# Kernel optimization log

Hardware: AMD Instinct MI355X
Metric: run time of the kernel (lower is better)

The kernel has to match this reference:

```python
import jax, jax.numpy as jnp
import numpy as np

ENCODER_STRIDE = 320
TEMPERATURE = 1.0


def setup_inputs() -> dict:
    key = jax.random.key(0)
    k1, k2, k3, k4 = jax.random.split(key, 4)
    B, D, T, K = 8, 512, 4096, 4096
    student_features = jax.random.normal(k1, (B, D, T), dtype=jnp.float32)
    codebook = jax.random.normal(k2, (K, D), dtype=jnp.float32)
    teacher_codes = jax.random.randint(k3, (B, T), 0, K, dtype=jnp.int64)
    lengths = jax.random.randint(k4, (B,), 0, T * ENCODER_STRIDE, dtype=jnp.int64)
    return {
        "student_features": student_features,
        "codebook": codebook,
        "teacher_codes": teacher_codes,
        "lengths": lengths,
    }


def reference(student_features, codebook, teacher_codes, lengths):
    B, D, T = student_features.shape
    # length mask over frames: frame t is valid if its start sample < length
    frame_starts = jnp.arange(T, dtype=jnp.int64) * ENCODER_STRIDE  # [T]
    mask = (frame_starts[None, :] < lengths[:, None]).astype(student_features.dtype)  # [B,T]

    z = jnp.transpose(student_features, (0, 2, 1)).reshape(-1, D)  # [N,D], N=B*T

    # cdist p=2: sqrt(|z|^2 + |c|^2 - 2 z.c)
    z2 = jnp.sum(z * z, axis=1, keepdims=True)            # [N,1]
    c2 = jnp.sum(codebook * codebook, axis=1)[None, :]    # [1,K]
    d2 = z2 + c2 - 2.0 * (z @ codebook.T)                 # [N,K]
    dists = jnp.sqrt(jnp.maximum(d2, 1e-12))

    soft_weights = jax.nn.softmax(-dists / TEMPERATURE, axis=1)  # [N,K]
    soft_recon = soft_weights @ codebook                          # [N,D]

    codes_flat = teacher_codes.reshape(-1)                        # [N]
    target_embeddings = jax.lax.stop_gradient(codebook[codes_flat])  # [N,D]

    diff_sq = jnp.mean((soft_recon - target_embeddings) ** 2, axis=1).reshape(B, T)
    loss = jnp.sum(diff_sq * mask) / (jnp.sum(mask) + 1e-8)
    return loss
```

## Files before the change

kernel.cpp:

```cpp
#include <hip/hip_runtime.h>
#include <hip/hip_bf16.h>


#define BB 8
#define DD 512
#define TT 4096
#define KKK 4096
#define ENC_STRIDE 320
#define KT 32
#define NKT (KKK / KT)
#define NW 8
#define ROWS 128
#define KBROW 2056
#define KBBYTES 4112
#define BUFB (8 * KBBYTES)

typedef __attribute__((ext_vector_type(8))) short bf16x8;
typedef __attribute__((ext_vector_type(4))) float f32x4;

union FragU { bf16x8 v; uint2 h2[2]; ushort us[8]; unsigned long long q[2]; uint4 u4; };

static __device__ __forceinline__ ushort f2bf(float x) {
  unsigned u = __float_as_uint(x);
  unsigned r = (u + 0x7FFFu + ((u >> 16) & 1u)) >> 16;
  return (ushort)r;
}
static __device__ __forceinline__ uint2 f4tobf(float4 v) {
  uint2 r;
  r.x = (unsigned)f2bf(v.x) | ((unsigned)f2bf(v.y) << 16);
  r.y = (unsigned)f2bf(v.z) | ((unsigned)f2bf(v.w) << 16);
  return r;
}
static __device__ __forceinline__ unsigned pk2bf(float lo, float hi) {
  return (__float_as_uint(lo) >> 16) | (__float_as_uint(hi) & 0xFFFF0000u);
}
static __device__ __forceinline__ void gld_lds16(const void* g, void* l) {
  __builtin_amdgcn_global_load_lds(
      (const __attribute__((address_space(1))) unsigned*)g,
      (__attribute__((address_space(3))) unsigned*)l, 16, 0, 0);
}
static __device__ __forceinline__ unsigned lds_addr(const void* p) {
  return (unsigned)(size_t)(const __attribute__((address_space(3))) char*)p;
}

__global__ __launch_bounds__(256) void vq_prep(const float* __restrict__ cb,
                                               float* __restrict__ c2,
                                               ushort* __restrict__ cbh) {
  int k = blockIdx.x * 4 + (threadIdx.x >> 6);
  int lane = threadIdx.x & 63;
  const float4* p = (const float4*)(cb + (size_t)k * DD + lane * 8);
  float4 a = p[0], b = p[1];
  if (cbh) {
    uint2 pa = f4tobf(a), pb = f4tobf(b);
    *(uint4*)(cbh + (size_t)k * DD + lane * 8) = make_uint4(pa.x, pa.y, pb.x, pb.y);
  }
  float s = a.x*a.x + a.y*a.y + a.z*a.z + a.w*a.w
          + b.x*b.x + b.y*b.y + b.z*b.z + b.w*b.w;
  #pragma unroll
  for (int m = 1; m <= 32; m <<= 1) s += __shfl_xor(s, m);
  if (lane == 0) c2[k] = s;
}

template <int GLD>
__global__ __launch_bounds__(512, 2) void vq_main(
    const float* __restrict__ sf,
    const float* __restrict__ cb,
    const ushort* __restrict__ cbh,
    const int*  __restrict__ codes,
    const int*  __restrict__ lens,
    const float* __restrict__ c2,
    float* __restrict__ num) {
  __shared__ __align__(128) ushort cs[4][8][KBROW];
  __shared__ __align__(16) ushort wlds[2][NW][16][40];
  __shared__ float  alds[2][ROWS];
  __shared__ float  llds[ROWS];
  __shared__ float  diffred[ROWS];
  __shared__ int    flagv[NKT];

  const int bid = blockIdx.x;
  const int b  = bid >> 5;
  const int t0 = (bid & 31) << 7;
  const int len = lens[b];
  int vcount = (len + (ENC_STRIDE - 1)) / ENC_STRIDE;
  vcount = vcount < TT ? vcount : TT;
  if (t0 >= vcount) return;

  const int tid = threadIdx.x;
  const int w  = tid >> 6;
  const int l  = tid & 63;
  const int lg = l >> 4;
  const int ln = l & 15;

  for (int i = tid; i < ROWS; i += 512) diffred[i] = 0.f;
  for (int i = tid; i < NKT; i += 512) flagv[i] = 0;

  const float* sfb = sf + (size_t)b * DD * TT;
  const int trow = t0 + w * 16 + ln;
  bf16x8 za[16];
  float z2 = 0.f;
  #pragma unroll
  for (int f = 0; f < 16; ++f) {
    #pragma unroll
    for (int j = 0; j < 8; ++j) {
      int d = f * 32 + lg * 8 + j;
      float v = sfb[(size_t)d * TT + trow];
      z2 += v * v;
      za[f][j] = (short)f2bf(v);
    }
  }
  z2 += __shfl_xor(z2, 16);
  z2 += __shfl_xor(z2, 32);

  const int sbase = (w * 4 + ((l >> 1) & 3)) * DD + (l >> 3) * 16 + (l & 1) * 8;
  auto stage = [&](int kt, int buf) {
    if (GLD) {
      const ushort* gb = cbh + (size_t)kt * KT * DD + sbase;
      ushort* lb = &cs[buf][w][0];
      #pragma unroll
      for (int q = 0; q < 4; ++q) gld_lds16(gb + q * 128, lb + q * 512);
    } else {
      const float* gb = cb + (size_t)kt * KT * DD + sbase;
      #pragma unroll
      for (int q = 0; q < 4; ++q) {
        float4 v0 = *(const float4*)(gb + q * 128);
        float4 v1 = *(const float4*)(gb + q * 128 + 4);
        uint2 a0 = f4tobf(v0), a1 = f4tobf(v1);
        *(uint4*)&cs[buf][w][q * 512 + l * 8] = make_uint4(a0.x, a0.y, a1.x, a1.y);
      }
    }
  };

  stage(0, 0); stage(1, 1); stage(2, 2);

  float mrow = -1e30f, lrow = 0.f;
  f32x4 acc[8][4];
  #pragma unroll
  for (int r = 0; r < 8; ++r)
    #pragma unroll
    for (int nt = 0; nt < 4; ++nt) acc[r][nt] = (f32x4){0.f, 0.f, 0.f, 0.f};

  const unsigned score_lane = (unsigned)((ln >> 2) * KBBYTES + (ln & 3) * 32
                                         + (lg >> 1) * 128 + (lg & 1) * 16);
  const unsigned tr_lane = (unsigned)(lg * KBBYTES + w * 512 + ln * 8);
  const unsigned cs0a = lds_addr(&cs[0][0][0]);

  f32x4 sc0, sc1;
  auto scores = [&](int it, int sbuf) {
    const char* csb = (const char*)&cs[sbuf][0][0];
    sc0 = (f32x4){0,0,0,0}; sc1 = (f32x4){0,0,0,0};
    __builtin_amdgcn_s_setprio(1);
    #pragma unroll
    for (int f = 0; f < 16; ++f) {
      bf16x8 a0 = *(const bf16x8*)(csb + score_lane + f * 256);
      bf16x8 a1 = *(const bf16x8*)(csb + score_lane + 16448 + f * 256);
      sc0 = __builtin_amdgcn_mfma_f32_16x16x32_bf16(a0, za[f], sc0, 0, 0, 0);
      sc1 = __builtin_amdgcn_mfma_f32_16x16x32_bf16(a1, za[f], sc1, 0, 0, 0);
    }
    __builtin_amdgcn_s_setprio(0);
  };

  __syncthreads();
  scores(0, 0);
  {
    const float4 c2a = *(const float4*)(c2 + lg * 4);
    const float4 c2b = *(const float4*)(c2 + 16 + lg * 4);
    float c2v[8] = {c2a.x, c2a.y, c2a.z, c2a.w, c2b.x, c2b.y, c2b.z, c2b.w};
    float sv[8];
    #pragma unroll
    for (int v = 0; v < 4; ++v) {
      sv[v]     = -sqrtf(fmaxf(z2 + c2v[v]     - 2.f * sc0[v], 1e-12f));
      sv[4 + v] = -sqrtf(fmaxf(z2 + c2v[4 + v] - 2.f * sc1[v], 1e-12f));
    }
    float lmax = sv[0];
    #pragma unroll
    for (int i = 1; i < 8; ++i) lmax = fmaxf(lmax, sv[i]);
    float tmax = fmaxf(lmax, __shfl_xor(lmax, 16));
    tmax = fmaxf(tmax, __shfl_xor(tmax, 32));
    float el[8], lsum = 0.f;
    #pragma unroll
    for (int i = 0; i < 8; ++i) { el[i] = __expf(sv[i] - lmax); lsum += el[i]; }
    mrow = tmax;
    float factor = __expf(lmax - tmax);
    float esum = lsum * factor;
    esum += __shfl_xor(esum, 16);
    esum += __shfl_xor(esum, 32);
    lrow = esum;
    uint4 pk;
    pk.x = pk2bf(el[0] * factor, el[1] * factor);
    pk.y = pk2bf(el[2] * factor, el[3] * factor);
    pk.z = pk2bf(el[4] * factor, el[5] * factor);
    pk.w = pk2bf(el[6] * factor, el[7] * factor);
    *(uint4*)&wlds[0][w][ln][lg * 8] = pk;
    if (lg == 0) alds[0][w * 16 + ln] = 1.f;
  }

  #pragma unroll 1
  for (int it = 1; it < NKT; ++it) {
    __syncthreads();
    if (it + 2 < NKT) stage(it + 2, (it + 2) & 3);

    scores(it, it & 3);

    const float4 c2a = *(const float4*)(c2 + it * KT + lg * 4);
    const float4 c2b = *(const float4*)(c2 + it * KT + 16 + lg * 4);
    float c2v[8] = {c2a.x, c2a.y, c2a.z, c2a.w, c2b.x, c2b.y, c2b.z, c2b.w};
    float sv[8];
    #pragma unroll
    for (int v = 0; v < 4; ++v) {
      sv[v]     = -sqrtf(fmaxf(z2 + c2v[v]     - 2.f * sc0[v], 1e-12f));
      sv[4 + v] = -sqrtf(fmaxf(z2 + c2v[4 + v] - 2.f * sc1[v], 1e-12f));
    }
    float lmax = sv[0];
    #pragma unroll
    for (int i = 1; i < 8; ++i) lmax = fmaxf(lmax, sv[i]);
    float el[8], lsum = 0.f;
    #pragma unroll
    for (int i = 0; i < 8; ++i) { el[i] = __expf(sv[i] - lmax); lsum += el[i]; }

    const int itm1 = it - 1;
    const int s = itm1 & 1;
    const unsigned trb = cs0a + (unsigned)(itm1 & 3) * BUFB + tr_lane;
    unsigned long long tq0[4], tq1[4];
    #pragma unroll
    for (int nt = 0; nt < 4; ++nt) {
      asm volatile("ds_read_b64_tr_b16 %0, %2 offset:%3\n\t"
                   "ds_read_b64_tr_b16 %1, %2 offset:%4"
                   : "=&v"(tq0[nt]), "=&v"(tq1[nt])
                   : "v"(trb), "i"(nt * 128), "i"(16448 + nt * 128));
    }

    float tmax = fmaxf(lmax, __shfl_xor(lmax, 16));
    tmax = fmaxf(tmax, __shfl_xor(tmax, 32));
    const bool defer = (tmax <= mrow + 8.f);
    const float mnew = defer ? mrow : tmax;
    const float factor = __expf(lmax - mnew);
    float esum = lsum * factor;
    esum += __shfl_xor(esum, 16);
    esum += __shfl_xor(esum, 32);
    const float alpha = defer ? 1.f : __expf(mrow - mnew);
    lrow = lrow * alpha + esum;
    mrow = mnew;
    uint4 pk;
    pk.x = pk2bf(el[0] * factor, el[1] * factor);
    pk.y = pk2bf(el[2] * factor, el[3] * factor);
    pk.z = pk2bf(el[4] * factor, el[5] * factor);
    pk.w = pk2bf(el[6] * factor, el[7] * factor);
    const int s2 = it & 1;
    *(uint4*)&wlds[s2][w][ln][lg * 8] = pk;
    if (lg == 0) alds[s2][w * 16 + ln] = alpha;
    if (!__all(defer) && l == 0) flagv[it] = 1;

    const int flg = flagv[itm1];
    asm volatile("s_waitcnt lgkmcnt(0)" ::: "memory");
    __builtin_amdgcn_sched_barrier(0);

    if (flg) {
      #pragma unroll
      for (int r = 0; r < 8; ++r)
        #pragma unroll
        for (int v = 0; v < 4; ++v) {
          float av = alds[s][r * 16 + lg * 4 + v];
          #pragma unroll
          for (int nt = 0; nt < 4; ++nt) acc[r][nt][v] *= av;
        }
    }
    FragU cf[4];
    #pragma unroll
    for (int nt = 0; nt < 4; ++nt) { cf[nt].q[0] = tq0[nt]; cf[nt].q[1] = tq1[nt]; }

    __builtin_amdgcn_s_setprio(1);
    #pragma unroll
    for (int rh = 0; rh < 2; ++rh) {
      bf16x8 wa4[4];
      #pragma unroll
      for (int r4 = 0; r4 < 4; ++r4)
        wa4[r4] = *(const bf16x8*)&wlds[s][rh * 4 + r4][ln][lg * 8];
      #pragma unroll
      for (int r4 = 0; r4 < 4; ++r4)
        #pragma unroll
        for (int nt = 0; nt < 4; ++nt)
          acc[rh * 4 + r4][nt] = __builtin_amdgcn_mfma_f32_16x16x32_bf16(
              wa4[r4], cf[nt].v, acc[rh * 4 + r4][nt], 0, 0, 0);
    }
    __builtin_amdgcn_s_setprio(0);
  }

  __syncthreads();
  {
    const int itm1 = NKT - 1;
    const int s = itm1 & 1;
    const unsigned trb = cs0a + (unsigned)(itm1 & 3) * BUFB + tr_lane;
    unsigned long long tq0[4], tq1[4];
    #pragma unroll
    for (int nt = 0; nt < 4; ++nt) {
      asm volatile("ds_read_b64_tr_b16 %0, %2 offset:%3\n\t"
                   "ds_read_b64_tr_b16 %1, %2 offset:%4"
                   : "=&v"(tq0[nt]), "=&v"(tq1[nt])
                   : "v"(trb), "i"(nt * 128), "i"(16448 + nt * 128));
    }
    const int flg = flagv[itm1];
    asm volatile("s_waitcnt lgkmcnt(0)" ::: "memory");
    __builtin_amdgcn_sched_barrier(0);
    if (flg) {
      #pragma unroll
      for (int r = 0; r < 8; ++r)
        #pragma unroll
        for (int v = 0; v < 4; ++v) {
          float av = alds[s][r * 16 + lg * 4 + v];
          #pragma unroll
          for (int nt = 0; nt < 4; ++nt) acc[r][nt][v] *= av;
        }
    }
    FragU cf[4];
    #pragma unroll
    for (int nt = 0; nt < 4; ++nt) { cf[nt].q[0] = tq0[nt]; cf[nt].q[1] = tq1[nt]; }
    #pragma unroll
    for (int rh = 0; rh < 2; ++rh) {
      bf16x8 wa4[4];
      #pragma unroll
      for (int r4 = 0; r4 < 4; ++r4)
        wa4[r4] = *(const bf16x8*)&wlds[s][rh * 4 + r4][ln][lg * 8];
      #pragma unroll
      for (int r4 = 0; r4 < 4; ++r4)
        #pragma unroll
        for (int nt = 0; nt < 4; ++nt)
          acc[rh * 4 + r4][nt] = __builtin_amdgcn_mfma_f32_16x16x32_bf16(
              wa4[r4], cf[nt].v, acc[rh * 4 + r4][nt], 0, 0, 0);
    }
  }

  if (lg == 0) llds[w * 16 + ln] = lrow;
  __syncthreads();
  const int* tcodes = codes + b * TT + t0;
  #pragma unroll
  for (int r = 0; r < 8; ++r) {
    float pv[4];
    #pragma unroll
    for (int v = 0; v < 4; ++v) {
      const int row = r * 16 + lg * 4 + v;
      const float lv = llds[row];
      const int tc = tcodes[row];
      const float* erow = cb + (size_t)tc * DD + w * 64;
      float ps = 0.f;
      #pragma unroll
      for (int nt = 0; nt < 4; ++nt) {
        float rc = acc[r][nt][v] / lv;
        float df = rc - erow[nt * 16 + ln];
        ps += df * df;
      }
      pv[v] = ps;
    }
    #pragma unroll
    for (int v = 0; v < 4; ++v) {
      pv[v] += __shfl_xor(pv[v], 1);
      pv[v] += __shfl_xor(pv[v], 2);
      pv[v] += __shfl_xor(pv[v], 4);
      pv[v] += __shfl_xor(pv[v], 8);
    }
    if (ln == 0) {
      #pragma unroll
      for (int v = 0; v < 4; ++v)
        atomicAdd(&diffred[r * 16 + lg * 4 + v], pv[v]);
    }
  }
  __syncthreads();
  if (tid < ROWS) {
    float val = (t0 + tid < vcount) ? diffred[tid] * (1.f / DD) : 0.f;
    val += __shfl_xor(val, 1);
    val += __shfl_xor(val, 2);
    val += __shfl_xor(val, 4);
    val += __shfl_xor(val, 8);
    val += __shfl_xor(val, 16);
    val += __shfl_xor(val, 32);
    if ((tid & 63) == 0) atomicAdd(num, val);
  }
}

__global__ void vq_finalize(const float* __restrict__ num,
                            const int* __restrict__ lens,
                            float* __restrict__ out) {
  float denom = 0.f;
  for (int b = 0; b < BB; ++b) {
    int v = (lens[b] + (ENC_STRIDE - 1)) / ENC_STRIDE;
    v = v < TT ? v : TT;
    denom += (float)v;
  }
  out[0] = num[0] / (denom + 1e-8f);
}

extern "C" void kernel_launch(void* const* d_in, const int* in_sizes, int n_in,
                              void* d_out, int out_size, void* d_ws, size_t ws_size,
                              hipStream_t stream) {
  const float* sf    = (const float*)d_in[0];
  const float* cb    = (const float*)d_in[1];
  const int*   codes = (const int*)d_in[2];
  const int*   lens  = (const int*)d_in[3];
  float* out = (float*)d_out;
  float* num = (float*)d_ws;
  float* c2  = (float*)((char*)d_ws + 256);
  const size_t need = 32768 + (size_t)KKK * DD * sizeof(ushort);
  ushort* cbh = (ws_size >= need) ? (ushort*)((char*)d_ws + 32768) : nullptr;

  hipMemsetAsync(d_ws, 0, 4, stream);
  vq_prep<<<KKK / 4, 256, 0, stream>>>(cb, c2, cbh);
  const int grid = (BB * TT) / ROWS;
  if (cbh)
    vq_main<1><<<grid, 512, 0, stream>>>(sf, cb, cbh, codes, lens, c2, num);
  else
    vq_main<0><<<grid, 512, 0, stream>>>(sf, cb, cbh, codes, lens, c2, num);
  vq_finalize<<<1, 1, 0, stream>>>(num, lens, out);
}
```

Before: 396.7 us.

## Split codebook dimension across blocks for balanced work over valid tiles

Adds a planning kernel that lists only the valid row tiles, then a persistent 256-block kernel that divides the flattened (row-tile × codebook-chunk) work evenly. Each block writes partial bf16 reconstructions plus per-row max and sum. A merge kernel then combines the partials with a log-sum-exp rescale and computes the masked loss. This targets load imbalance and idle CUs, since the old grid launched one block per 128-row tile and skipped masked tiles unevenly. In exchange it adds two kernel launches, a large workspace round trip of partial results, and extra bf16 rounding of the partial reconstructions.

```diff
diff --git a/kernel.cpp b/kernel.cpp
--- a/kernel.cpp
+++ b/kernel.cpp
@@ -15,6 +15,13 @@
 #define KBBYTES 4112
 #define BUFB (8 * KBBYTES)
 
+#define WS_C2    256
+#define WS_RTS   16640
+#define WS_CBH   32768
+#define WS_PART  4227072ULL
+#define WS_ML    (WS_PART + 67108864ULL)
+#define WS_NEED  (WS_ML + 524288ULL)
+
 typedef __attribute__((ext_vector_type(8))) short bf16x8;
 typedef __attribute__((ext_vector_type(4))) float f32x4;
 
@@ -33,6 +40,9 @@
 }
 static __device__ __forceinline__ unsigned pk2bf(float lo, float hi) {
   return (__float_as_uint(lo) >> 16) | (__float_as_uint(hi) & 0xFFFF0000u);
+}
+static __device__ __forceinline__ float bfh2f(ushort h) {
+  return __uint_as_float(((unsigned)h) << 16);
 }
 static __device__ __forceinline__ void gld_lds16(const void* g, void* l) {
   __builtin_amdgcn_global_load_lds(
@@ -61,14 +71,406 @@
   if (lane == 0) c2[k] = s;
 }
 
+__global__ void vq_plan(const int* __restrict__ lens, int* __restrict__ hdr,
+                        int* __restrict__ rts) {
+  int n = 0;
+  for (int b2 = 0; b2 < BB; ++b2) {
+    int v = (lens[b2] + (ENC_STRIDE - 1)) / ENC_STRIDE;
+    v = v < TT ? v : TT;
+    int tiles = (v + 127) >> 7;
+    for (int t = 0; t < tiles; ++t) rts[n++] = (b2 << 5) | t;
+  }
+  hdr[0] = n;
+  hdr[1] = (n * 128 + 255) >> 8;
+  hdr[2] = n * 128;
+}
+
+__global__ __launch_bounds__(512, 2) void vq_main_ws(
+    const float* __restrict__ sf,
+    const ushort* __restrict__ cbh,
+    const float* __restrict__ c2,
+    const int* __restrict__ hdr,
+    const int* __restrict__ rts,
+    ushort* __restrict__ recon_p,
+    float* __restrict__ ml) {
+  __shared__ __align__(128) ushort cs[4][8][KBROW];
+  __shared__ __align__(16) ushort wlds[2][NW][16][40];
+  __shared__ float  alds[2][ROWS];
+  __shared__ float  llds[ROWS];
+  __shared__ int    flagv[128];
+
+  const int Q = hdr[1], total = hdr[2];
+  int start = blockIdx.x * Q;
+  if (Q == 0 || start >= total) return;
+  int end = start + Q;
+  end = end < total ? end : total;
+  int slot = blockIdx.x * 2;
+
+  const int tid = threadIdx.x;
+  const int w  = tid >> 6;
+  const int l  = tid & 63;
+  const int lg = l >> 4;
+  const int ln = l & 15;
+  const int sbase = (w * 4 + ((l >> 1) & 3)) * DD + (l >> 3) * 16 + (l & 1) * 8;
+  const unsigned score_lane = (unsigned)((ln >> 2) * KBBYTES + (ln & 3) * 32
+                                         + (lg >> 1) * 128 + (lg & 1) * 16);
+  const unsigned tr_lane = (unsigned)(lg * KBBYTES + w * 512 + ln * 8);
+  const unsigned cs0a = lds_addr(&cs[0][0][0]);
+
+  while (start < end) {
+    const int rt = start >> 7;
+    const int k0 = start & 127;
+    int seg_end = (rt + 1) << 7;
+    seg_end = seg_end < end ? seg_end : end;
+    const int klen = seg_end - start;
+    const int rtv = rts[rt];
+    const int b  = rtv >> 5;
+    const int t0 = (rtv & 31) << 7;
+
+    for (int i2 = tid; i2 < klen; i2 += 512) flagv[i2] = 0;
+
+    const float* sfb = sf + (size_t)b * DD * TT;
+    const int trow = t0 + w * 16 + ln;
+    bf16x8 za[16];
+    float z2 = 0.f;
+    #pragma unroll
+    for (int f = 0; f < 16; ++f) {
+      #pragma unroll
+      for (int j = 0; j < 8; ++j) {
+        int d = f * 32 + lg * 8 + j;
+        float v = sfb[(size_t)d * TT + trow];
+        z2 += v * v;
+        za[f][j] = (short)f2bf(v);
+      }
+    }
+    z2 += __shfl_xor(z2, 16);
+    z2 += __shfl_xor(z2, 32);
+
+    auto stage = [&](int kta, int buf) {
+      const ushort* gb = cbh + (size_t)kta * KT * DD + sbase;
+      ushort* lb = &cs[buf][w][0];
+      #pragma unroll
+      for (int q = 0; q < 4; ++q) gld_lds16(gb + q * 128, lb + q * 512);
+    };
+
+    stage(k0, 0);
+    if (klen > 1) stage(k0 + 1, 1);
+    if (klen > 2) stage(k0 + 2, 2);
+
+    float mrow = -1e30f, lrow = 0.f;
+    f32x4 acc[8][4];
+    #pragma unroll
+    for (int r = 0; r < 8; ++r)
+      #pragma unroll
+      for (int nt = 0; nt < 4; ++nt) acc[r][nt] = (f32x4){0.f, 0.f, 0.f, 0.f};
+
+    f32x4 sc0, sc1;
+    auto scores = [&](int sbuf) {
+      const char* csb = (const char*)&cs[sbuf][0][0];
+      sc0 = (f32x4){0,0,0,0}; sc1 = (f32x4){0,0,0,0};
+      __builtin_amdgcn_s_setprio(1);
+      #pragma unroll
+      for (int f = 0; f < 16; ++f) {
+        bf16x8 a0 = *(const bf16x8*)(csb + score_lane + f * 256);
+        bf16x8 a1 = *(const bf16x8*)(csb + score_lane + 16448 + f * 256);
+        sc0 = __builtin_amdgcn_mfma_f32_16x16x32_bf16(a0, za[f], sc0, 0, 0, 0);
+        sc1 = __builtin_amdgcn_mfma_f32_16x16x32_bf16(a1, za[f], sc1, 0, 0, 0);
+      }
+      __builtin_amdgcn_s_setprio(0);
+    };
+
+    __syncthreads();
+    scores(0);
+    {
+      const float4 c2a = *(const float4*)(c2 + k0 * KT + lg * 4);
+      const float4 c2b = *(const float4*)(c2 + k0 * KT + 16 + lg * 4);
+      float c2v[8] = {c2a.x, c2a.y, c2a.z, c2a.w, c2b.x, c2b.y, c2b.z, c2b.w};
+      float sv[8];
+      #pragma unroll
+      for (int v = 0; v < 4; ++v) {
+        sv[v]     = -sqrtf(fmaxf(z2 + c2v[v]     - 2.f * sc0[v], 1e-12f));
+        sv[4 + v] = -sqrtf(fmaxf(z2 + c2v[4 + v] - 2.f * sc1[v], 1e-12f));
+      }
+      float lmax = sv[0];
+      #pragma unroll
+      for (int i = 1; i < 8; ++i) lmax = fmaxf(lmax, sv[i]);
+      float tmax = fmaxf(lmax, __shfl_xor(lmax, 16));
+      tmax = fmaxf(tmax, __shfl_xor(tmax, 32));
+      float el[8], lsum = 0.f;
+      #pragma unroll
+      for (int i = 0; i < 8; ++i) { el[i] = __expf(sv[i] - lmax); lsum += el[i]; }
+      mrow = tmax;
+      float factor = __expf(lmax - tmax);
+      float esum = lsum * factor;
+      esum += __shfl_xor(esum, 16);
+      esum += __shfl_xor(esum, 32);
+      lrow = esum;
+      uint4 pk;
+      pk.x = pk2bf(el[0] * factor, el[1] * factor);
+      pk.y = pk2bf(el[2] * factor, el[3] * factor);
+      pk.z = pk2bf(el[4] * factor, el[5] * factor);
+      pk.w = pk2bf(el[6] * factor, el[7] * factor);
+      *(uint4*)&wlds[0][w][ln][lg * 8] = pk;
+      if (lg == 0) alds[0][w * 16 + ln] = 1.f;
+    }
+
+    #pragma unroll 1
+    for (int li = 1; li < klen; ++li) {
+      __syncthreads();
+      if (li + 2 < klen) stage(k0 + li + 2, (li + 2) & 3);
+
+      scores(li & 3);
+
+      const int kta = k0 + li;
+      const float4 c2a = *(const float4*)(c2 + kta * KT + lg * 4);
+      const float4 c2b = *(const float4*)(c2 + kta * KT + 16 + lg * 4);
+      float c2v[8] = {c2a.x, c2a.y, c2a.z, c2a.w, c2b.x, c2b.y, c2b.z, c2b.w};
+      float sv[8];
+      #pragma unroll
+      for (int v = 0; v < 4; ++v) {
+        sv[v]     = -sqrtf(fmaxf(z2 + c2v[v]     - 2.f * sc0[v], 1e-12f));
+        sv[4 + v] = -sqrtf(fmaxf(z2 + c2v[4 + v] - 2.f * sc1[v], 1e-12f));
+      }
+      float lmax = sv[0];
+      #pragma unroll
+      for (int i = 1; i < 8; ++i) lmax = fmaxf(lmax, sv[i]);
+      float el[8], lsum = 0.f;
+      #pragma unroll
+      for (int i = 0; i < 8; ++i) { el[i] = __expf(sv[i] - lmax); lsum += el[i]; }
+
+      const int lim1 = li - 1;
+      const int s = lim1 & 1;
+      const unsigned trb = cs0a + (unsigned)(lim1 & 3) * BUFB + tr_lane;
+      unsigned long long tq0[4], tq1[4];
+      #pragma unroll
+      for (int nt = 0; nt < 4; ++nt) {
+        asm volatile("ds_read_b64_tr_b16 %0, %2 offset:%3\n\t"
+                     "ds_read_b64_tr_b16 %1, %2 offset:%4"
+                     : "=&v"(tq0[nt]), "=&v"(tq1[nt])
+                     : "v"(trb), "i"(nt * 128), "i"(16448 + nt * 128));
+      }
+
+      float tmax = fmaxf(lmax, __shfl_xor(lmax, 16));
+      tmax = fmaxf(tmax, __shfl_xor(tmax, 32));
+      const bool defer = (tmax <= mrow + 8.f);
+      const float mnew = defer ? mrow : tmax;
+      const float factor = __expf(lmax - mnew);
+      float esum = lsum * factor;
+      esum += __shfl_xor(esum, 16);
+      esum += __shfl_xor(esum, 32);
+      const float alpha = defer ? 1.f : __expf(mrow - mnew);
+      lrow = lrow * alpha + esum;
+      mrow = mnew;
+      uint4 pk;
+      pk.x = pk2bf(el[0] * factor, el[1] * factor);
+      pk.y = pk2bf(el[2] * factor, el[3] * factor);
+      pk.z = pk2bf(el[4] * factor, el[5] * factor);
+      pk.w = pk2bf(el[6] * factor, el[7] * factor);
+      const int s2 = li & 1;
+      *(uint4*)&wlds[s2][w][ln][lg * 8] = pk;
+      if (lg == 0) alds[s2][w * 16 + ln] = alpha;
+      if (!__all(defer) && l == 0) flagv[li] = 1;
+
+      const int flg = flagv[lim1];
+      asm volatile("s_waitcnt lgkmcnt(0)" ::: "memory");
+      __builtin_amdgcn_sched_barrier(0);
+
+      if (flg) {
+        #pragma unroll
+        for (int r = 0; r < 8; ++r)
+          #pragma unroll
+          for (int v = 0; v < 4; ++v) {
+            float av = alds[s][r * 16 + lg * 4 + v];
+            #pragma unroll
+            for (int nt = 0; nt < 4; ++nt) acc[r][nt][v] *= av;
+          }
+      }
+      FragU cf[4];
+      #pragma unroll
+      for (int nt = 0; nt < 4; ++nt) { cf[nt].q[0] = tq0[nt]; cf[nt].q[1] = tq1[nt]; }
+
+      __builtin_amdgcn_s_setprio(1);
+      #pragma unroll
+      for (int rh = 0; rh < 2; ++rh) {
+        bf16x8 wa4[4];
+        #pragma unroll
+        for (int r4 = 0; r4 < 4; ++r4)
+          wa4[r4] = *(const bf16x8*)&wlds[s][rh * 4 + r4][ln][lg * 8];
+        #pragma unroll
+        for (int r4 = 0; r4 < 4; ++r4)
+          #pragma unroll
+          for (int nt = 0; nt < 4; ++nt)
+            acc[rh * 4 + r4][nt] = __builtin_amdgcn_mfma_f32_16x16x32_bf16(
+                wa4[r4], cf[nt].v, acc[rh * 4 + r4][nt], 0, 0, 0);
+      }
+      __builtin_amdgcn_s_setprio(0);
+    }
+
+    __syncthreads();
+    {
+      const int lim1 = klen - 1;
+      const int s = lim1 & 1;
+      const unsigned trb = cs0a + (unsigned)(lim1 & 3) * BUFB + tr_lane;
+      unsigned long long tq0[4], tq1[4];
+      #pragma unroll
+      for (int nt = 0; nt < 4; ++nt) {
+        asm volatile("ds_read_b64_tr_b16 %0, %2 offset:%3\n\t"
+                     "ds_read_b64_tr_b16 %1, %2 offset:%4"
+                     : "=&v"(tq0[nt]), "=&v"(tq1[nt])
+                     : "v"(trb), "i"(nt * 128), "i"(16448 + nt * 128));
+      }
+      const int flg = flagv[lim1];
+      asm volatile("s_waitcnt lgkmcnt(0)" ::: "memory");
+      __builtin_amdgcn_sched_barrier(0);
+      if (flg) {
+        #pragma unroll
+        for (int r = 0; r < 8; ++r)
+          #pragma unroll
+          for (int v = 0; v < 4; ++v) {
+            float av = alds[s][r * 16 + lg * 4 + v];
+            #pragma unroll
+            for (int nt = 0; nt < 4; ++nt) acc[r][nt][v] *= av;
+          }
+      }
+      FragU cf[4];
+      #pragma unroll
+      for (int nt = 0; nt < 4; ++nt) { cf[nt].q[0] = tq0[nt]; cf[nt].q[1] = tq1[nt]; }
+      #pragma unroll
+      for (int rh = 0; rh < 2; ++rh) {
+        bf16x8 wa4[4];
+        #pragma unroll
+        for (int r4 = 0; r4 < 4; ++r4)
+          wa4[r4] = *(const bf16x8*)&wlds[s][rh * 4 + r4][ln][lg * 8];
+        #pragma unroll
+        for (int r4 = 0; r4 < 4; ++r4)
+          #pragma unroll
+          for (int nt = 0; nt < 4; ++nt)
+            acc[rh * 4 + r4][nt] = __builtin_amdgcn_mfma_f32_16x16x32_bf16(
+                wa4[r4], cf[nt].v, acc[rh * 4 + r4][nt], 0, 0, 0);
+      }
+    }
+
+    if (lg == 0) {
+      llds[w * 16 + ln] = lrow;
+      float2 mlv; mlv.x = mrow; mlv.y = lrow;
+      *(float2*)&ml[(size_t)(slot * 128 + w * 16 + ln) * 2] = mlv;
+    }
+    __syncthreads();
+    {
+      ushort* rp = recon_p + (size_t)slot * (128 * 512);
+      #pragma unroll
+      for (int r = 0; r < 8; ++r) {
+        #pragma unroll
+        for (int v = 0; v < 4; ++v) {
+          const int row = r * 16 + lg * 4 + v;
+          const float lv = llds[row];
+          #pragma unroll
+          for (int nt = 0; nt < 4; ++nt) {
+            const int d = w * 64 + nt * 16 + ln;
+            rp[row * 512 + d] = f2bf(acc[r][nt][v] / lv);
+          }
+        }
+      }
+    }
+    __syncthreads();
+
+    start += klen;
+    slot++;
+  }
+}
+
+__global__ __launch_bounds__(512) void vq_merge(
+    const ushort* __restrict__ recon_p, const float* __restrict__ ml,
+    const int* __restrict__ hdr, const int* __restrict__ rts,
+    const int* __restrict__ lens, const float* __restrict__ cb,
+    const int* __restrict__ codes, float* __restrict__ num) {
+  __shared__ float red[128];
+  const int i = blockIdx.x;
+  const int nact = hdr[0];
+  if (i >= nact) return;
+  const int Q = hdr[1], total = hdr[2];
+  const int rtv = rts[i];
+  const int b = rtv >> 5;
+  const int t0 = (rtv & 31) << 7;
+  int vcount = (lens[b] + (ENC_STRIDE - 1)) / ENC_STRIDE;
+  vcount = vcount < TT ? vcount : TT;
+
+  const int tid = threadIdx.x;
+  const int r = tid >> 2;
+  const int q = tid & 3;
+  const int flat0 = i << 7, flat1 = flat0 + 128;
+  int c_lo = flat0 / Q;
+  int c_hi = (flat1 - 1) / Q;
+  c_hi = c_hi < 255 ? c_hi : 255;
+
+  float M = -1e30f;
+  for (int c = c_lo; c <= c_hi; ++c) {
+    const int cs_ = c * Q;
+    int ce = cs_ + Q; ce = ce < total ? ce : total;
+    if (cs_ >= flat1 || ce <= flat0) continue;
+    const int slot = c * 2 + (i - (cs_ >> 7));
+    M = fmaxf(M, ml[(size_t)(slot * 128 + r) * 2]);
+  }
+  float L = 0.f;
+  for (int c = c_lo; c <= c_hi; ++c) {
+    const int cs_ = c * Q;
+    int ce = cs_ + Q; ce = ce < total ? ce : total;
+    if (cs_ >= flat1 || ce <= flat0) continue;
+    const int slot = c * 2 + (i - (cs_ >> 7));
+    const float m_ = ml[(size_t)(slot * 128 + r) * 2];
+    const float l_ = ml[(size_t)(slot * 128 + r) * 2 + 1];
+    L += l_ * __expf(m_ - M);
+  }
+  const float invL = 1.f / L;
+
+  const int tc = codes[b * TT + t0 + r];
+  const float* targ = cb + (size_t)tc * DD + q * 128;
+
+  float psum = 0.f;
+  #pragma unroll 1
+  for (int ch = 0; ch < 16; ++ch) {
+    const int d0 = q * 128 + ch * 8;
+    float rec[8] = {0.f, 0.f, 0.f, 0.f, 0.f, 0.f, 0.f, 0.f};
+    for (int c = c_lo; c <= c_hi; ++c) {
+      const int cs_ = c * Q;
+      int ce = cs_ + Q; ce = ce < total ? ce : total;
+      if (cs_ >= flat1 || ce <= flat0) continue;
+      const int slot = c * 2 + (i - (cs_ >> 7));
+      const float m_ = ml[(size_t)(slot * 128 + r) * 2];
+      const float l_ = ml[(size_t)(slot * 128 + r) * 2 + 1];
+      const float wn = l_ * __expf(m_ - M) * invL;
+      const ushort* rp = recon_p + (size_t)slot * (128 * 512) + r * 512 + d0;
+      FragU u; u.u4 = *(const uint4*)rp;
+      #pragma unroll
+      for (int j = 0; j < 8; ++j) rec[j] += wn * bfh2f(u.us[j]);
+    }
+    const float4 tg0 = *(const float4*)(targ + ch * 8);
+    const float4 tg1 = *(const float4*)(targ + ch * 8 + 4);
+    float tg[8] = {tg0.x, tg0.y, tg0.z, tg0.w, tg1.x, tg1.y, tg1.z, tg1.w};
+    #pragma unroll
+    for (int j = 0; j < 8; ++j) { float df = rec[j] - tg[j]; psum += df * df; }
+  }
+  psum += __shfl_xor(psum, 1);
+  psum += __shfl_xor(psum, 2);
+  if (q == 0) red[r] = ((t0 + r) < vcount) ? psum * (1.f / DD) : 0.f;
+  __syncthreads();
+  if (tid < 128) {
+    float val = red[tid];
+    val += __shfl_xor(val, 1);
+    val += __shfl_xor(val, 2);
+    val += __shfl_xor(val, 4);
+    val += __shfl_xor(val, 8);
+    val += __shfl_xor(val, 16);
+    val += __shfl_xor(val, 32);
+    if ((tid & 63) == 0) atomicAdd(num, val);
+  }
+}
+
 template <int GLD>
 __global__ __launch_bounds__(512, 2) void vq_main(
-    const float* __restrict__ sf,
-    const float* __restrict__ cb,
-    const ushort* __restrict__ cbh,
-    const int*  __restrict__ codes,
-    const int*  __restrict__ lens,
-    const float* __restrict__ c2,
+    const float* __restrict__ sf, const float* __restrict__ cb,
+    const ushort* __restrict__ cbh, const int* __restrict__ codes,
+    const int* __restrict__ lens, const float* __restrict__ c2,
     float* __restrict__ num) {
   __shared__ __align__(128) ushort cs[4][8][KBROW];
   __shared__ __align__(16) ushort wlds[2][NW][16][40];
@@ -198,7 +600,6 @@
   for (int it = 1; it < NKT; ++it) {
     __syncthreads();
     if (it + 2 < NKT) stage(it + 2, (it + 2) & 3);
-
     scores(it, it & 3);
 
     const float4 c2a = *(const float4*)(c2 + it * KT + lg * 4);
@@ -397,16 +798,27 @@
   const int*   lens  = (const int*)d_in[3];
   float* out = (float*)d_out;
   float* num = (float*)d_ws;
-  float* c2  = (float*)((char*)d_ws + 256);
-  const size_t need = 32768 + (size_t)KKK * DD * sizeof(ushort);
-  ushort* cbh = (ws_size >= need) ? (ushort*)((char*)d_ws + 32768) : nullptr;
+  int*   hdr = (int*)((char*)d_ws + 16);
+  float* c2  = (float*)((char*)d_ws + WS_C2);
+  int*   rts = (int*)((char*)d_ws + WS_RTS);
+  const size_t need_gld = WS_CBH + (size_t)KKK * DD * sizeof(ushort);
+  ushort* cbh = (ws_size >= need_gld) ? (ushort*)((char*)d_ws + WS_CBH) : nullptr;
 
   hipMemsetAsync(d_ws, 0, 4, stream);
   vq_prep<<<KKK / 4, 256, 0, stream>>>(cb, c2, cbh);
-  const int grid = (BB * TT) / ROWS;
-  if (cbh)
-    vq_main<1><<<grid, 512, 0, stream>>>(sf, cb, cbh, codes, lens, c2, num);
-  else
-    vq_main<0><<<grid, 512, 0, stream>>>(sf, cb, cbh, codes, lens, c2, num);
+
+  if (cbh && ws_size >= WS_NEED) {
+    ushort* recon_p = (ushort*)((char*)d_ws + WS_PART);
+    float*  mlp     = (float*)((char*)d_ws + WS_ML);
+    vq_plan<<<1, 1, 0, stream>>>(lens, hdr, rts);
+    vq_main_ws<<<256, 512, 0, stream>>>(sf, cbh, c2, hdr, rts, recon_p, mlp);
+    vq_merge<<<256, 512, 0, stream>>>(recon_p, mlp, hdr, rts, lens, cb, codes, num);
+  } else {
+    const int grid = (BB * TT) / ROWS;
+    if (cbh)
+      vq_main<1><<<grid, 512, 0, stream>>>(sf, cb, cbh, codes, lens, c2, num);
+    else
+      vq_main<0><<<grid, 512, 0, stream>>>(sf, cb, cbh, codes, lens, c2, num);
+  }
   vq_finalize<<<1, 1, 0, stream>>>(num, lens, out);
 }
```

Measured after the change: 380.7 us. 4.0% less time.
